# Kernel tuning notes

Measured on AMD Instinct MI355X. Metric: run time of the kernel, lower is better.

## Reference

```python
import jax, jax.numpy as jnp
import numpy as np

N_NODES = 100000
N_EDGES = 1600000
D_IN, D_HID, D_OUT = 128, 256, 128


def setup_inputs() -> dict:
    key = jax.random.key(0)
    ks = jax.random.split(key, 9)
    s = lambda d: 1.0 / np.sqrt(d)
    x = jax.random.normal(ks[0], (N_NODES, D_IN), dtype=jnp.float32)
    edge_index = jax.random.randint(ks[1], (2, N_EDGES), 0, N_NODES, dtype=jnp.int64)
    return {
        "x": x,
        "edge_index": edge_index,
        "Wl1": jax.random.normal(ks[2], (D_IN, D_HID), jnp.float32) * s(D_IN),
        "Wr1": jax.random.normal(ks[3], (D_IN, D_HID), jnp.float32) * s(D_IN),
        "b1": jnp.zeros((D_HID,), jnp.float32),
        "Wl2": jax.random.normal(ks[4], (D_HID, D_HID), jnp.float32) * s(D_HID),
        "Wr2": jax.random.normal(ks[5], (D_HID, D_HID), jnp.float32) * s(D_HID),
        "b2": jnp.zeros((D_HID,), jnp.float32),
        "Wl3": jax.random.normal(ks[6], (D_HID, D_OUT), jnp.float32) * s(D_HID),
        "Wr3": jax.random.normal(ks[7], (D_HID, D_OUT), jnp.float32) * s(D_HID),
        "b3": jnp.zeros((D_OUT,), jnp.float32),
    }


def _sage_conv(x, src, dst, Wl, Wr, b):
    # PyG SAGEConv (mean aggr): out = lin_l(mean_{j in N(i)} x_j) + lin_r(x_i)
    msg = x[src]                                                  # [E, d] gather
    agg = jax.ops.segment_sum(msg, dst, num_segments=N_NODES)    # [N, d] scatter-add
    cnt = jax.ops.segment_sum(jnp.ones((src.shape[0],), x.dtype), dst,
                              num_segments=N_NODES)
    mean = agg / jnp.maximum(cnt, 1.0)[:, None]
    return mean @ Wl + x @ Wr + b


def reference(x, edge_index, Wl1, Wr1, b1, Wl2, Wr2, b2, Wl3, Wr3, b3):
    src, dst = edge_index[0], edge_index[1]
    h = jax.nn.relu(_sage_conv(x, src, dst, Wl1, Wr1, b1))
    h = jax.nn.relu(_sage_conv(h, src, dst, Wl2, Wr2, b2))
    h = jax.nn.relu(_sage_conv(h, src, dst, Wl3, Wr3, b3))
    return h
```

## Files before the change

### kernel.cpp

```cpp
#include <hip/hip_runtime.h>
#include <hip/hip_bf16.h>

#define N_NODES 100000
#define NBUK 391
#define CHUNK 4096

typedef unsigned short ushort_t;
typedef unsigned char uchar_t;
typedef __attribute__((ext_vector_type(8))) short bf16x8;
typedef __attribute__((ext_vector_type(4))) float f32x4;
typedef __attribute__((ext_vector_type(2))) float f32x2;

__device__ inline float bfbits2f(unsigned int lo16) { return __uint_as_float(lo16 << 16); }

__device__ inline ushort_t f2bfbits(float f) {
    __hip_bfloat16 h = __float2bfloat16(f);
    return *reinterpret_cast<ushort_t*>(&h);
}

__device__ inline unsigned int pk2bf(float lo, float hi) {
    return (unsigned int)f2bfbits(lo) | ((unsigned int)f2bfbits(hi) << 16);
}

__device__ inline uchar_t f2fp8(float f) {
    int p = __builtin_amdgcn_cvt_pk_fp8_f32(f, 0.0f, 0, false);
    return (uchar_t)(p & 0xff);
}

__device__ inline void acc8_fp8(float* a, unsigned int ux, unsigned int uy) {
    f32x2 f01 = __builtin_amdgcn_cvt_pk_f32_fp8(ux, false);
    f32x2 f23 = __builtin_amdgcn_cvt_pk_f32_fp8(ux, true);
    f32x2 f45 = __builtin_amdgcn_cvt_pk_f32_fp8(uy, false);
    f32x2 f67 = __builtin_amdgcn_cvt_pk_f32_fp8(uy, true);
    a[0] += f01.x; a[1] += f01.y; a[2] += f23.x; a[3] += f23.y;
    a[4] += f45.x; a[5] += f45.y; a[6] += f67.x; a[7] += f67.y;
}

__device__ inline void acc16_fp8(float* a, uint4 u) {
    acc8_fp8(a, u.x, u.y);
    acc8_fp8(a + 8, u.z, u.w);
}

__global__ __launch_bounds__(256) void scan1(const int* __restrict__ in, int* __restrict__ out,
                                             int* __restrict__ bsum, int n) {
    __shared__ int lds[256];
    const int t = threadIdx.x;
    const int base = blockIdx.x * 1024 + t * 4;
    int4 v = {0, 0, 0, 0};
    if (base + 3 < n) v = *(const int4*)(in + base);
    else {
        v.x = (base + 0 < n) ? in[base + 0] : 0;
        v.y = (base + 1 < n) ? in[base + 1] : 0;
        v.z = (base + 2 < n) ? in[base + 2] : 0;
        v.w = (base + 3 < n) ? in[base + 3] : 0;
    }
    int s0 = v.x, s1 = s0 + v.y, s2 = s1 + v.z, s3 = s2 + v.w;
    lds[t] = s3;
    __syncthreads();
    for (int off = 1; off < 256; off <<= 1) {
        int a = (t >= off) ? lds[t - off] : 0;
        __syncthreads();
        lds[t] += a;
        __syncthreads();
    }
    const int texcl = lds[t] - s3;
    if (t == 255) bsum[blockIdx.x] = lds[255];
    if (base + 0 < n) out[base + 0] = texcl;
    if (base + 1 < n) out[base + 1] = texcl + s0;
    if (base + 2 < n) out[base + 2] = texcl + s1;
    if (base + 3 < n) out[base + 3] = texcl + s2;
}

__global__ __launch_bounds__(256) void scan2(int* __restrict__ bsum, int nb) {
    __shared__ int lds[256];
    const int t = threadIdx.x;
    int v = (t < nb) ? bsum[t] : 0;
    lds[t] = v;
    __syncthreads();
    for (int off = 1; off < 256; off <<= 1) {
        int a = (t >= off) ? lds[t - off] : 0;
        __syncthreads();
        lds[t] += a;
        __syncthreads();
    }
    if (t < nb) bsum[t] = lds[t] - v;
}

__global__ void scan3(int* __restrict__ out, const int* __restrict__ bsum, int n, int E) {
    int i = blockIdx.x * blockDim.x + threadIdx.x;
    if (i < n) out[i] += bsum[i >> 10];
    if (i == 0) out[n] = E;
}

__global__ __launch_bounds__(256) void hist1(const int* __restrict__ dst, int* __restrict__ H,
                                             int E, int NC) {
    __shared__ int h[NBUK + 1];
    const int t = threadIdx.x, c = blockIdx.x;
    for (int g = t; g <= NBUK; g += 256) h[g] = 0;
    __syncthreads();
    const long base = (long)c * CHUNK;
#pragma unroll 4
    for (int it = 0; it < CHUNK / 256; ++it) {
        long e = base + it * 256 + t;
        if (e < E) atomicAdd(&h[((unsigned)dst[e]) >> 8], 1);
    }
    __syncthreads();
    for (int g = t; g < NBUK; g += 256) H[(size_t)g * NC + c] = h[g];
}

__global__ __launch_bounds__(256) void binA(const int* __restrict__ src,
                                            const int* __restrict__ dst,
                                            const int* __restrict__ Hs,
                                            uint2* __restrict__ tmp, int E, int NC) {
    __shared__ int cur[NBUK + 1];
    const int t = threadIdx.x, c = blockIdx.x;
    for (int g = t; g < NBUK; g += 256) cur[g] = Hs[(size_t)g * NC + c];
    __syncthreads();
    const long cb = (long)c * CHUNK;
#pragma unroll 4
    for (int it = 0; it < CHUNK / 256; ++it) {
        long e = cb + it * 256 + t;
        if (e < E) {
            unsigned d = (unsigned)dst[e];
            int pos = atomicAdd(&cur[d >> 8], 1);
            uint2 p = {d, (unsigned)src[e]};
            tmp[pos] = p;
        }
    }
}

__global__ __launch_bounds__(256) void hist2_inv(const uint2* __restrict__ tmp,
                                                 const int* __restrict__ Hs,
                                                 int* __restrict__ cnt,
                                                 float* __restrict__ invd, int NC) {
    __shared__ int h[256];
    const int t = threadIdx.x, b = blockIdx.x;
    h[t] = 0;
    __syncthreads();
    const int beg = Hs[(size_t)b * NC], end = Hs[(size_t)(b + 1) * NC];
    for (int e = beg + t; e < end; e += 256) atomicAdd(&h[tmp[e].x & 255u], 1);
    __syncthreads();
    const int d = b * 256 + t;
    if (d < N_NODES) {
        cnt[d] = h[t];
        invd[d] = 1.0f / (float)max(h[t], 1);
    }
}

__global__ __launch_bounds__(256) void scatter2(const uint2* __restrict__ tmp,
                                                const int* __restrict__ Hs,
                                                const int* __restrict__ roff,
                                                int* __restrict__ csr, int NC) {
    __shared__ int cur[256];
    const int t = threadIdx.x, b = blockIdx.x;
    const int d = b * 256 + t;
    cur[t] = (d <= N_NODES) ? roff[min(d, N_NODES)] : 0;
    __syncthreads();
    const int beg = Hs[(size_t)b * NC], end = Hs[(size_t)(b + 1) * NC];
    for (int e = beg + t; e < end; e += 256) {
        uint2 p = tmp[e];
        int pos = atomicAdd(&cur[p.x & 255u], 1);
        csr[pos] = (int)p.y;
    }
}

__global__ void round_both(const float* __restrict__ x, ushort_t* __restrict__ xb,
                           uchar_t* __restrict__ x8, long n) {
    long i = ((long)blockIdx.x * blockDim.x + threadIdx.x) * 4;
    if (i < n) {
        float4 v = *(const float4*)(x + i);
        ushort4 o = {f2bfbits(v.x), f2bfbits(v.y), f2bfbits(v.z), f2bfbits(v.w)};
        *(ushort4*)(xb + i) = o;
        int w = __builtin_amdgcn_cvt_pk_fp8_f32(v.x, v.y, 0, false);
        w = __builtin_amdgcn_cvt_pk_fp8_f32(v.z, v.w, w, true);
        *(unsigned int*)(x8 + i) = (unsigned int)w;
    }
}

__global__ void cvt_transpose(const float* __restrict__ W, ushort_t* __restrict__ WT,
                              int K, int J, int kdst0, int ldwt) {
    int idx = blockIdx.x * blockDim.x + threadIdx.x;
    if (idx >= K * J) return;
    int k = idx / J, j = idx - k * J;
    WT[(size_t)j * ldwt + kdst0 + k] = f2bfbits(W[idx]);
}

__global__ void cvt6(const float* __restrict__ Wl2, const float* __restrict__ Wr2,
                     const float* __restrict__ Wl3, const float* __restrict__ Wr3,
                     ushort_t* __restrict__ WT2A, ushort_t* __restrict__ WT2B,
                     ushort_t* __restrict__ WT3) {
    const int y = blockIdx.y;
    int idx = blockIdx.x * blockDim.x + threadIdx.x;
    if (idx >= 256 * 128) return;
    int k = idx >> 7, jj = idx & 127;
    const float* W;
    ushort_t* WT;
    int J = 256, jsrc0 = 0;
    switch (y) {
        case 0: W = Wl2; WT = WT2A; break;
        case 1: W = Wr2; WT = WT2A; break;
        case 2: W = Wl2; WT = WT2B; jsrc0 = 128; break;
        case 3: W = Wr2; WT = WT2B; jsrc0 = 128; break;
        case 4: W = Wl3; WT = WT3; J = 128; break;
        default: W = Wr3; WT = WT3; J = 128; break;
    }
    const int row0 = (y & 1) * 128;
    WT[(size_t)(row0 + jj) * 256 + k] = f2bfbits(W[(size_t)k * J + jsrc0 + jj]);
}

template <bool ADDZ, typename OT>
__global__ __launch_bounds__(256) void gather_mean(const uchar_t* __restrict__ Y,
                                                   const ushort_t* __restrict__ Z,
                                                   const int* __restrict__ roff,
                                                   const int* __restrict__ csr,
                                                   const float* __restrict__ invd,
                                                   OT* __restrict__ out, int out_ld, int col0) {
    const int w = (blockIdx.x * blockDim.x + threadIdx.x) >> 6;
    if (w >= N_NODES) return;
    const int lane = threadIdx.x & 63;
    const int g = lane >> 4;
    const int l = lane & 15;
    const int e0 = roff[w], e1 = roff[w + 1];

    float a[8] = {0.f, 0.f, 0.f, 0.f, 0.f, 0.f, 0.f, 0.f};

    int e = e0 + g;
    for (; e + 12 < e1; e += 16) {
        const int s0 = csr[e], s1 = csr[e + 4], s2 = csr[e + 8], s3 = csr[e + 12];
        uint2 u0 = *(const uint2*)(Y + (size_t)s0 * 128 + l * 8);
        uint2 u1 = *(const uint2*)(Y + (size_t)s1 * 128 + l * 8);
        uint2 u2 = *(const uint2*)(Y + (size_t)s2 * 128 + l * 8);
        uint2 u3 = *(const uint2*)(Y + (size_t)s3 * 128 + l * 8);
        acc8_fp8(a, u0.x, u0.y); acc8_fp8(a, u1.x, u1.y);
        acc8_fp8(a, u2.x, u2.y); acc8_fp8(a, u3.x, u3.y);
    }
    for (; e < e1; e += 4) {
        uint2 u0 = *(const uint2*)(Y + (size_t)csr[e] * 128 + l * 8);
        acc8_fp8(a, u0.x, u0.y);
    }

#pragma unroll
    for (int i = 0; i < 8; ++i) {
        a[i] += __shfl_xor(a[i], 16);
        a[i] += __shfl_xor(a[i], 32);
    }

    if (g != 0) return;
    const float iv = invd[w];
#pragma unroll
    for (int i = 0; i < 8; ++i) a[i] *= iv;

    if constexpr (ADDZ) {
        uint4 z = *(const uint4*)(Z + (size_t)w * 128 + l * 8);
        float zf[8];
        zf[0] = bfbits2f(z.x & 0xffffu); zf[1] = __uint_as_float(z.x & 0xffff0000u);
        zf[2] = bfbits2f(z.y & 0xffffu); zf[3] = __uint_as_float(z.y & 0xffff0000u);
        zf[4] = bfbits2f(z.z & 0xffffu); zf[5] = __uint_as_float(z.z & 0xffff0000u);
        zf[6] = bfbits2f(z.w & 0xffffu); zf[7] = __uint_as_float(z.w & 0xffff0000u);
#pragma unroll
        for (int i = 0; i < 8; ++i) a[i] = fmaxf(a[i] + zf[i], 0.0f);
    }

    if constexpr (sizeof(OT) == 4) {
        float* op = (float*)out + (size_t)w * out_ld + col0 + l * 8;
        float4 s0 = {a[0], a[1], a[2], a[3]};
        float4 s1 = {a[4], a[5], a[6], a[7]};
        *(float4*)op = s0;
        *(float4*)(op + 4) = s1;
    } else {
        ushort_t* op = (ushort_t*)out + (size_t)w * out_ld + col0 + l * 8;
        ushort4 lohi0 = {f2bfbits(a[0]), f2bfbits(a[1]), f2bfbits(a[2]), f2bfbits(a[3])};
        ushort4 lohi1 = {f2bfbits(a[4]), f2bfbits(a[5]), f2bfbits(a[6]), f2bfbits(a[7])};
        *(ushort4*)op = lohi0;
        *(ushort4*)(op + 4) = lohi1;
    }
}

__global__ __launch_bounds__(256) void gather256(const uchar_t* __restrict__ Y,
                                                 const ushort_t* __restrict__ Z,
                                                 const int* __restrict__ roff,
                                                 const int* __restrict__ csr,
                                                 const float* __restrict__ invd,
                                                 ushort_t* __restrict__ out) {
    const int w = (blockIdx.x * blockDim.x + threadIdx.x) >> 6;
    if (w >= N_NODES) return;
    const int lane = threadIdx.x & 63;
    const int g = lane >> 4;
    const int l = lane & 15;
    const int e0 = roff[w], e1 = roff[w + 1];

    float a[16];
#pragma unroll
    for (int i = 0; i < 16; ++i) a[i] = 0.0f;

    int e = e0 + g;
    for (; e + 12 < e1; e += 16) {
        const int s0 = csr[e], s1 = csr[e + 4], s2 = csr[e + 8], s3 = csr[e + 12];
        uint4 u0 = *(const uint4*)(Y + (size_t)s0 * 256 + l * 16);
        uint4 u1 = *(const uint4*)(Y + (size_t)s1 * 256 + l * 16);
        uint4 u2 = *(const uint4*)(Y + (size_t)s2 * 256 + l * 16);
        uint4 u3 = *(const uint4*)(Y + (size_t)s3 * 256 + l * 16);
        acc16_fp8(a, u0); acc16_fp8(a, u1); acc16_fp8(a, u2); acc16_fp8(a, u3);
    }
    for (; e < e1; e += 4) {
        uint4 u0 = *(const uint4*)(Y + (size_t)csr[e] * 256 + l * 16);
        acc16_fp8(a, u0);
    }

#pragma unroll
    for (int i = 0; i < 16; ++i) {
        a[i] += __shfl_xor(a[i], 16);
        a[i] += __shfl_xor(a[i], 32);
    }

    if (g != 0) return;
    const float iv = invd[w];

    uint4 z0 = *(const uint4*)(Z + (size_t)w * 256 + l * 16);
    uint4 z1 = *(const uint4*)(Z + (size_t)w * 256 + l * 16 + 8);
    float zf[16];
    zf[0] = bfbits2f(z0.x & 0xffffu);  zf[1] = __uint_as_float(z0.x & 0xffff0000u);
    zf[2] = bfbits2f(z0.y & 0xffffu);  zf[3] = __uint_as_float(z0.y & 0xffff0000u);
    zf[4] = bfbits2f(z0.z & 0xffffu);  zf[5] = __uint_as_float(z0.z & 0xffff0000u);
    zf[6] = bfbits2f(z0.w & 0xffffu);  zf[7] = __uint_as_float(z0.w & 0xffff0000u);
    zf[8] = bfbits2f(z1.x & 0xffffu);  zf[9] = __uint_as_float(z1.x & 0xffff0000u);
    zf[10] = bfbits2f(z1.y & 0xffffu); zf[11] = __uint_as_float(z1.y & 0xffff0000u);
    zf[12] = bfbits2f(z1.z & 0xffffu); zf[13] = __uint_as_float(z1.z & 0xffff0000u);
    zf[14] = bfbits2f(z1.w & 0xffffu); zf[15] = __uint_as_float(z1.w & 0xffff0000u);

#pragma unroll
    for (int i = 0; i < 16; ++i) a[i] = fmaxf(a[i] * iv + zf[i], 0.0f);

    ushort_t* op = out + (size_t)w * 256 + l * 16;
    uint4 s0, s1;
    s0.x = pk2bf(a[0], a[1]);   s0.y = pk2bf(a[2], a[3]);
    s0.z = pk2bf(a[4], a[5]);   s0.w = pk2bf(a[6], a[7]);
    s1.x = pk2bf(a[8], a[9]);   s1.y = pk2bf(a[10], a[11]);
    s1.z = pk2bf(a[12], a[13]); s1.w = pk2bf(a[14], a[15]);
    *(uint4*)op = s0;
    *(uint4*)(op + 8) = s1;
}

template <int KH, bool CONCAT, int MODE>
__global__ __launch_bounds__(256) void mfma_gemm256(const ushort_t* __restrict__ A,
                                                    const ushort_t* __restrict__ A2,
                                                    const ushort_t* __restrict__ WT,
                                                    const float* __restrict__ bias,
                                                    void* __restrict__ out0p, int ld0,
                                                    ushort_t* __restrict__ out1, int ld1) {
    constexpr int KTOT = CONCAT ? 2 * KH : KH;
    constexpr int BK = 32;
    constexpr int NT = KTOT / BK;
    __shared__ ushort_t smem[2][12288];

    const int tid = threadIdx.x;
    const int lane = tid & 63;
    const int w = tid >> 6;
    const int wr = w >> 1, wc = w & 1;
    const int n0 = blockIdx.x * 128;

    const int srow = lane >> 2;
    const int skc = (lane & 3) ^ ((srow >> 1) & 3);

    f32x4 acc0[4][4], acc1[4][4];
#pragma unroll
    for (int m = 0; m < 4; ++m)
#pragma unroll
        for (int n = 0; n < 4; ++n) {
            acc0[m][n] = (f32x4){0.f, 0.f, 0.f, 0.f};
            acc1[m][n] = (f32x4){0.f, 0.f, 0.f, 0.f};
        }

    auto STAGE = [&](int b, int t) {
        const int k0 = t * BK;
        const ushort_t* Asrc = A;
        int ak = k0;
        if (CONCAT && k0 >= KH) { Asrc = A2; ak = k0 - KH; }
#pragma unroll
        for (int i = 0; i < 2; ++i) {
            const int ci = w * 2 + i;
            int grow = n0 + ci * 16 + srow;
            grow = min(grow, N_NODES - 1);
            const ushort_t* g = Asrc + (size_t)grow * KH + ak + skc * 8;
            __builtin_amdgcn_global_load_lds((const unsigned int*)g,
                                             (unsigned int*)(&smem[b][ci * 512]), 16, 0, 0);
        }
#pragma unroll
        for (int i = 0; i < 4; ++i) {
            const int ci = w * 4 + i;
            const int jrow = ci * 16 + srow;
            const ushort_t* g = WT + (size_t)jrow * KTOT + k0 + skc * 8;
            __builtin_amdgcn_global_load_lds((const unsigned int*)g,
                                             (unsigned int*)(&smem[b][4096 + ci * 512]), 16, 0, 0);
        }
    };

    auto COMPUTE = [&](int b) {
        const int kc = lane >> 4;
        bf16x8 af[4], b0[4], b1[4];
#pragma unroll
        for (int m = 0; m < 4; ++m) {
            const int row = wr * 64 + m * 16 + (lane & 15);
            const int slot = kc ^ ((row >> 1) & 3);
            af[m] = *(const bf16x8*)((const char*)&smem[b][0] + row * 64 + slot * 16);
        }
#pragma unroll
        for (int n = 0; n < 4; ++n) {
            const int r0 = wc * 64 + n * 16 + (lane & 15);
            const int r1 = 128 + r0;
            const int s0 = kc ^ ((r0 >> 1) & 3);
            const int s1 = kc ^ ((r1 >> 1) & 3);
            b0[n] = *(const bf16x8*)((const char*)&smem[b][4096] + r0 * 64 + s0 * 16);
            b1[n] = *(const bf16x8*)((const char*)&smem[b][4096] + r1 * 64 + s1 * 16);
        }
#pragma unroll
        for (int m = 0; m < 4; ++m)
#pragma unroll
            for (int n = 0; n < 4; ++n) {
                acc0[m][n] = __builtin_amdgcn_mfma_f32_16x16x32_bf16(af[m], b0[n],
                                                                     acc0[m][n], 0, 0, 0);
                acc1[m][n] = __builtin_amdgcn_mfma_f32_16x16x32_bf16(af[m], b1[n],
                                                                     acc1[m][n], 0, 0, 0);
            }
    };

    STAGE(0, 0);
    __syncthreads();
    int cur = 0;
#pragma unroll
    for (int t = 0; t < NT - 1; ++t) {
        STAGE(cur ^ 1, t + 1);
        COMPUTE(cur);
        __syncthreads();
        cur ^= 1;
    }
    COMPUTE(cur);

    const int c15 = lane & 15;
    const int r4 = (lane >> 4) * 4;
#pragma unroll
    for (int m = 0; m < 4; ++m) {
#pragma unroll
        for (int q = 0; q < 4; ++q) {
            const int row_g = n0 + wr * 64 + m * 16 + r4 + q;
            if (row_g >= N_NODES) continue;
#pragma unroll
            for (int n = 0; n < 4; ++n) {
                const int lcol = wc * 64 + n * 16 + c15;
                const float v0 = acc0[m][n][q];
                const float v1 = acc1[m][n][q];
                if constexpr (MODE == 0) {
                    ushort_t* o = (ushort_t*)out0p;
                    o[(size_t)row_g * ld0 + lcol] = f2bfbits(fmaxf(v0 + bias[lcol], 0.0f));
                    o[(size_t)row_g * ld0 + 128 + lcol] =
                        f2bfbits(fmaxf(v1 + bias[128 + lcol], 0.0f));
                } else {
                    ((uchar_t*)out0p)[(size_t)row_g * ld0 + lcol] = f2fp8(v0);
                    out1[(size_t)row_g * ld1 + lcol] = f2bfbits(v1 + bias[lcol]);
                }
            }
        }
    }
}

extern "C" void kernel_launch(void* const* d_in, const int* in_sizes, int n_in,
                              void* d_out, int out_size, void* d_ws, size_t ws_size,
                              hipStream_t stream) {
    const float* x   = (const float*)d_in[0];
    const int*   ei  = (const int*)d_in[1];
    const float* Wl1 = (const float*)d_in[2];
    const float* Wr1 = (const float*)d_in[3];
    const float* b1  = (const float*)d_in[4];
    const float* Wl2 = (const float*)d_in[5];
    const float* Wr2 = (const float*)d_in[6];
    const float* b2  = (const float*)d_in[7];
    const float* Wl3 = (const float*)d_in[8];
    const float* Wr3 = (const float*)d_in[9];
    const float* b3  = (const float*)d_in[10];

    const int E = in_sizes[1] / 2;
    const int* src = ei;
    const int* dst = ei + E;
    const int N = N_NODES;
    const int NC = (E + CHUNK - 1) / CHUNK;
    const int nH = NBUK * NC;

    char* ws = (char*)d_ws;
    float* invd = (float*)(ws + 0);
    int* cnt    = (int*)(ws + 400000);
    int* roff   = (int*)(ws + 800000);
    int* bsum   = (int*)(ws + 1200016);
    int* H      = (int*)(ws + 1201040);
    ushort_t* WT1  = (ushort_t*)(ws + 1812568);
    ushort_t* WT2A = (ushort_t*)(ws + 1943640);
    ushort_t* WT2B = (ushort_t*)(ws + 2074712);
    ushort_t* WT3  = (ushort_t*)(ws + 2205784);
    uint2* tmp  = (uint2*)(ws + 2336864);
    int* csr    = (int*)(ws + 15136864);
    ushort_t* h1 = (ushort_t*)(ws + 21536864);
    ushort_t* h2 = (ushort_t*)(ws + 72736864);
    ushort_t* M1 = h2;
    ushort_t* T1 = (ushort_t*)(ws + 123936864);
    const size_t WS_NEED = 149536864;
    if (ws_size < WS_NEED) return;

    uchar_t* T8  = (uchar_t*)tmp;
    uchar_t* T1a = (uchar_t*)T1;
    ushort_t* Zd = (ushort_t*)d_out;
    ushort_t* Zh = h1;

    const int GX = (N + 127) / 128;
    const int NBH = (nH + 1023) / 1024;
    const int NBN = (N + 1023) / 1024;

    hist1<<<NC, 256, 0, stream>>>(dst, H, E, NC);
    scan1<<<NBH, 256, 0, stream>>>(H, H, bsum, nH);
    scan2<<<1, 256, 0, stream>>>(bsum, NBH);
    scan3<<<(nH + 256) / 256, 256, 0, stream>>>(H, bsum, nH, E);
    binA<<<NC, 256, 0, stream>>>(src, dst, H, tmp, E, NC);
    hist2_inv<<<NBUK, 256, 0, stream>>>(tmp, H, cnt, invd, NC);
    scan1<<<NBN, 256, 0, stream>>>(cnt, roff, bsum, N);
    scan2<<<1, 256, 0, stream>>>(bsum, NBN);
    scan3<<<(N + 256) / 256, 256, 0, stream>>>(roff, bsum, N, E);
    scatter2<<<NBUK, 256, 0, stream>>>(tmp, H, roff, csr, NC);

    cvt_transpose<<<(128 * 256 + 255) / 256, 256, 0, stream>>>(Wl1, WT1, 128, 256, 0, 256);
    cvt_transpose<<<(128 * 256 + 255) / 256, 256, 0, stream>>>(Wr1, WT1, 128, 256, 128, 256);
    cvt6<<<dim3(128, 6), 256, 0, stream>>>(Wl2, Wr2, Wl3, Wr3, WT2A, WT2B, WT3);

    round_both<<<(N * 128 / 4 + 255) / 256, 256, 0, stream>>>(x, T1, T8, (long)N * 128);
    gather_mean<false, ushort_t><<<(N * 64 + 255) / 256, 256, 0, stream>>>(
        T8, nullptr, roff, csr, invd, M1, 128, 0);
    mfma_gemm256<128, true, 0><<<GX, 256, 0, stream>>>(
        M1, T1, WT1, b1, h1, 256, nullptr, 0);

    mfma_gemm256<256, false, 1><<<GX, 256, 0, stream>>>(
        h1, nullptr, WT2A, b2 + 0, T1a, 256, Zd, 256);
    mfma_gemm256<256, false, 1><<<GX, 256, 0, stream>>>(
        h1, nullptr, WT2B, b2 + 128, T1a + 128, 256, Zd + 128, 256);
    gather256<<<(N * 64 + 255) / 256, 256, 0, stream>>>(
        T1a, Zd, roff, csr, invd, h2);

    mfma_gemm256<256, false, 1><<<GX, 256, 0, stream>>>(
        h2, nullptr, WT3, b3, T8, 128, Zh, 128);
    gather_mean<true, float><<<(N * 64 + 255) / 256, 256, 0, stream>>>(
        T8, Zh, roff, csr, invd, (float*)d_out, 128, 0);
}
```

Before: 447.4 us.

## Split neighbor gathers into 32-column slices processed by interleaved blocks

Replaces the per-node gather kernels with one templated kernel in which each wavefront handles a 32-byte column slice of a node, and consecutive blocks cover the different slices of the same node group. The intent is to shrink each pass's working set, so concurrent blocks touching the same slice share cache lines in L2/MALL and gather locality improves. The cost is more wavefronts, with every slice re-reading the CSR indices and offsets. Each lane now issues small 4-byte loads, and a third shuffle-reduction step is added.

```diff
diff --git a/kernel.cpp b/kernel.cpp
--- a/kernel.cpp
+++ b/kernel.cpp
@@ -18,27 +18,15 @@
     return *reinterpret_cast<ushort_t*>(&h);
 }
 
-__device__ inline unsigned int pk2bf(float lo, float hi) {
-    return (unsigned int)f2bfbits(lo) | ((unsigned int)f2bfbits(hi) << 16);
-}
-
 __device__ inline uchar_t f2fp8(float f) {
     int p = __builtin_amdgcn_cvt_pk_fp8_f32(f, 0.0f, 0, false);
     return (uchar_t)(p & 0xff);
 }
 
-__device__ inline void acc8_fp8(float* a, unsigned int ux, unsigned int uy) {
-    f32x2 f01 = __builtin_amdgcn_cvt_pk_f32_fp8(ux, false);
-    f32x2 f23 = __builtin_amdgcn_cvt_pk_f32_fp8(ux, true);
-    f32x2 f45 = __builtin_amdgcn_cvt_pk_f32_fp8(uy, false);
-    f32x2 f67 = __builtin_amdgcn_cvt_pk_f32_fp8(uy, true);
+__device__ inline void acc4_fp8(float* a, unsigned int u) {
+    f32x2 f01 = __builtin_amdgcn_cvt_pk_f32_fp8(u, false);
+    f32x2 f23 = __builtin_amdgcn_cvt_pk_f32_fp8(u, true);
     a[0] += f01.x; a[1] += f01.y; a[2] += f23.x; a[3] += f23.y;
-    a[4] += f45.x; a[5] += f45.y; a[6] += f67.x; a[7] += f67.y;
-}
-
-__device__ inline void acc16_fp8(float* a, uint4 u) {
-    acc8_fp8(a, u.x, u.y);
-    acc8_fp8(a + 8, u.z, u.w);
 }
 
 __global__ __launch_bounds__(256) void scan1(const int* __restrict__ in, int* __restrict__ out,
@@ -208,137 +196,69 @@
     WT[(size_t)(row0 + jj) * 256 + k] = f2bfbits(W[(size_t)k * J + jsrc0 + jj]);
 }
 
-template <bool ADDZ, typename OT>
-__global__ __launch_bounds__(256) void gather_mean(const uchar_t* __restrict__ Y,
-                                                   const ushort_t* __restrict__ Z,
-                                                   const int* __restrict__ roff,
-                                                   const int* __restrict__ csr,
-                                                   const float* __restrict__ invd,
-                                                   OT* __restrict__ out, int out_ld, int col0) {
-    const int w = (blockIdx.x * blockDim.x + threadIdx.x) >> 6;
-    if (w >= N_NODES) return;
-    const int lane = threadIdx.x & 63;
-    const int g = lane >> 4;
-    const int l = lane & 15;
-    const int e0 = roff[w], e1 = roff[w + 1];
-
-    float a[8] = {0.f, 0.f, 0.f, 0.f, 0.f, 0.f, 0.f, 0.f};
-
-    int e = e0 + g;
-    for (; e + 12 < e1; e += 16) {
-        const int s0 = csr[e], s1 = csr[e + 4], s2 = csr[e + 8], s3 = csr[e + 12];
-        uint2 u0 = *(const uint2*)(Y + (size_t)s0 * 128 + l * 8);
-        uint2 u1 = *(const uint2*)(Y + (size_t)s1 * 128 + l * 8);
-        uint2 u2 = *(const uint2*)(Y + (size_t)s2 * 128 + l * 8);
-        uint2 u3 = *(const uint2*)(Y + (size_t)s3 * 128 + l * 8);
-        acc8_fp8(a, u0.x, u0.y); acc8_fp8(a, u1.x, u1.y);
-        acc8_fp8(a, u2.x, u2.y); acc8_fp8(a, u3.x, u3.y);
-    }
-    for (; e < e1; e += 4) {
-        uint2 u0 = *(const uint2*)(Y + (size_t)csr[e] * 128 + l * 8);
-        acc8_fp8(a, u0.x, u0.y);
-    }
-
-#pragma unroll
-    for (int i = 0; i < 8; ++i) {
-        a[i] += __shfl_xor(a[i], 16);
-        a[i] += __shfl_xor(a[i], 32);
-    }
-
-    if (g != 0) return;
-    const float iv = invd[w];
-#pragma unroll
-    for (int i = 0; i < 8; ++i) a[i] *= iv;
-
-    if constexpr (ADDZ) {
-        uint4 z = *(const uint4*)(Z + (size_t)w * 128 + l * 8);
-        float zf[8];
-        zf[0] = bfbits2f(z.x & 0xffffu); zf[1] = __uint_as_float(z.x & 0xffff0000u);
-        zf[2] = bfbits2f(z.y & 0xffffu); zf[3] = __uint_as_float(z.y & 0xffff0000u);
-        zf[4] = bfbits2f(z.z & 0xffffu); zf[5] = __uint_as_float(z.z & 0xffff0000u);
-        zf[6] = bfbits2f(z.w & 0xffffu); zf[7] = __uint_as_float(z.w & 0xffff0000u);
-#pragma unroll
-        for (int i = 0; i < 8; ++i) a[i] = fmaxf(a[i] + zf[i], 0.0f);
-    }
-
-    if constexpr (sizeof(OT) == 4) {
-        float* op = (float*)out + (size_t)w * out_ld + col0 + l * 8;
-        float4 s0 = {a[0], a[1], a[2], a[3]};
-        float4 s1 = {a[4], a[5], a[6], a[7]};
-        *(float4*)op = s0;
-        *(float4*)(op + 4) = s1;
-    } else {
-        ushort_t* op = (ushort_t*)out + (size_t)w * out_ld + col0 + l * 8;
-        ushort4 lohi0 = {f2bfbits(a[0]), f2bfbits(a[1]), f2bfbits(a[2]), f2bfbits(a[3])};
-        ushort4 lohi1 = {f2bfbits(a[4]), f2bfbits(a[5]), f2bfbits(a[6]), f2bfbits(a[7])};
-        *(ushort4*)op = lohi0;
-        *(ushort4*)(op + 4) = lohi1;
-    }
-}
-
-__global__ __launch_bounds__(256) void gather256(const uchar_t* __restrict__ Y,
+template <int NCOLS, bool ADDZ, typename OT>
+__global__ __launch_bounds__(256) void gather_sl(const uchar_t* __restrict__ Y,
                                                  const ushort_t* __restrict__ Z,
                                                  const int* __restrict__ roff,
                                                  const int* __restrict__ csr,
                                                  const float* __restrict__ invd,
-                                                 ushort_t* __restrict__ out) {
-    const int w = (blockIdx.x * blockDim.x + threadIdx.x) >> 6;
-    if (w >= N_NODES) return;
+                                                 OT* __restrict__ out) {
+    const int bx = blockIdx.x;
+    const int s8 = bx & 7;
+    int slice, ng;
+    if (NCOLS == 256) { slice = s8; ng = bx >> 3; }
+    else { slice = s8 & 3; ng = ((bx >> 3) << 1) | (s8 >> 2); }
+
+    const int node = ng * 4 + (threadIdx.x >> 6);
+    if (node >= N_NODES) return;
     const int lane = threadIdx.x & 63;
-    const int g = lane >> 4;
-    const int l = lane & 15;
-    const int e0 = roff[w], e1 = roff[w + 1];
-
-    float a[16];
-#pragma unroll
-    for (int i = 0; i < 16; ++i) a[i] = 0.0f;
+    const int g = lane >> 3;
+    const int li = lane & 7;
+    const int e0 = roff[node], e1 = roff[node + 1];
+    const size_t coff = (size_t)slice * 32 + li * 4;
+
+    float a[4] = {0.f, 0.f, 0.f, 0.f};
 
     int e = e0 + g;
-    for (; e + 12 < e1; e += 16) {
-        const int s0 = csr[e], s1 = csr[e + 4], s2 = csr[e + 8], s3 = csr[e + 12];
-        uint4 u0 = *(const uint4*)(Y + (size_t)s0 * 256 + l * 16);
-        uint4 u1 = *(const uint4*)(Y + (size_t)s1 * 256 + l * 16);
-        uint4 u2 = *(const uint4*)(Y + (size_t)s2 * 256 + l * 16);
-        uint4 u3 = *(const uint4*)(Y + (size_t)s3 * 256 + l * 16);
-        acc16_fp8(a, u0); acc16_fp8(a, u1); acc16_fp8(a, u2); acc16_fp8(a, u3);
-    }
-    for (; e < e1; e += 4) {
-        uint4 u0 = *(const uint4*)(Y + (size_t)csr[e] * 256 + l * 16);
-        acc16_fp8(a, u0);
-    }
-
-#pragma unroll
-    for (int i = 0; i < 16; ++i) {
+    for (; e + 8 < e1; e += 16) {
+        unsigned int u0 = *(const unsigned int*)(Y + (size_t)csr[e] * NCOLS + coff);
+        unsigned int u1 = *(const unsigned int*)(Y + (size_t)csr[e + 8] * NCOLS + coff);
+        acc4_fp8(a, u0);
+        acc4_fp8(a, u1);
+    }
+    if (e < e1) {
+        unsigned int u0 = *(const unsigned int*)(Y + (size_t)csr[e] * NCOLS + coff);
+        acc4_fp8(a, u0);
+    }
+
+#pragma unroll
+    for (int i = 0; i < 4; ++i) {
+        a[i] += __shfl_xor(a[i], 8);
         a[i] += __shfl_xor(a[i], 16);
         a[i] += __shfl_xor(a[i], 32);
     }
 
     if (g != 0) return;
-    const float iv = invd[w];
-
-    uint4 z0 = *(const uint4*)(Z + (size_t)w * 256 + l * 16);
-    uint4 z1 = *(const uint4*)(Z + (size_t)w * 256 + l * 16 + 8);
-    float zf[16];
-    zf[0] = bfbits2f(z0.x & 0xffffu);  zf[1] = __uint_as_float(z0.x & 0xffff0000u);
-    zf[2] = bfbits2f(z0.y & 0xffffu);  zf[3] = __uint_as_float(z0.y & 0xffff0000u);
-    zf[4] = bfbits2f(z0.z & 0xffffu);  zf[5] = __uint_as_float(z0.z & 0xffff0000u);
-    zf[6] = bfbits2f(z0.w & 0xffffu);  zf[7] = __uint_as_float(z0.w & 0xffff0000u);
-    zf[8] = bfbits2f(z1.x & 0xffffu);  zf[9] = __uint_as_float(z1.x & 0xffff0000u);
-    zf[10] = bfbits2f(z1.y & 0xffffu); zf[11] = __uint_as_float(z1.y & 0xffff0000u);
-    zf[12] = bfbits2f(z1.z & 0xffffu); zf[13] = __uint_as_float(z1.z & 0xffff0000u);
-    zf[14] = bfbits2f(z1.w & 0xffffu); zf[15] = __uint_as_float(z1.w & 0xffff0000u);
-
-#pragma unroll
-    for (int i = 0; i < 16; ++i) a[i] = fmaxf(a[i] * iv + zf[i], 0.0f);
-
-    ushort_t* op = out + (size_t)w * 256 + l * 16;
-    uint4 s0, s1;
-    s0.x = pk2bf(a[0], a[1]);   s0.y = pk2bf(a[2], a[3]);
-    s0.z = pk2bf(a[4], a[5]);   s0.w = pk2bf(a[6], a[7]);
-    s1.x = pk2bf(a[8], a[9]);   s1.y = pk2bf(a[10], a[11]);
-    s1.z = pk2bf(a[12], a[13]); s1.w = pk2bf(a[14], a[15]);
-    *(uint4*)op = s0;
-    *(uint4*)(op + 8) = s1;
+    const float iv = invd[node];
+#pragma unroll
+    for (int i = 0; i < 4; ++i) a[i] *= iv;
+
+    if constexpr (ADDZ) {
+        uint2 z = *(const uint2*)(Z + (size_t)node * NCOLS + slice * 32 + li * 4);
+        float zf[4];
+        zf[0] = bfbits2f(z.x & 0xffffu); zf[1] = __uint_as_float(z.x & 0xffff0000u);
+        zf[2] = bfbits2f(z.y & 0xffffu); zf[3] = __uint_as_float(z.y & 0xffff0000u);
+#pragma unroll
+        for (int i = 0; i < 4; ++i) a[i] = fmaxf(a[i] + zf[i], 0.0f);
+    }
+
+    if constexpr (sizeof(OT) == 4) {
+        float4 st = {a[0], a[1], a[2], a[3]};
+        *(float4*)((float*)out + (size_t)node * 128 + slice * 32 + li * 4) = st;
+    } else {
+        ushort4 st = {f2bfbits(a[0]), f2bfbits(a[1]), f2bfbits(a[2]), f2bfbits(a[3])};
+        *(ushort4*)((ushort_t*)out + (size_t)node * NCOLS + slice * 32 + li * 4) = st;
+    }
 }
 
 template <int KH, bool CONCAT, int MODE>
@@ -512,6 +432,8 @@
     const int GX = (N + 127) / 128;
     const int NBH = (nH + 1023) / 1024;
     const int NBN = (N + 1023) / 1024;
+    const int G128 = 8 * ((N + 7) / 8);
+    const int G256 = 8 * ((N + 3) / 4);
 
     hist1<<<NC, 256, 0, stream>>>(dst, H, E, NC);
     scan1<<<NBH, 256, 0, stream>>>(H, H, bsum, nH);
@@ -529,8 +451,8 @@
     cvt6<<<dim3(128, 6), 256, 0, stream>>>(Wl2, Wr2, Wl3, Wr3, WT2A, WT2B, WT3);
 
     round_both<<<(N * 128 / 4 + 255) / 256, 256, 0, stream>>>(x, T1, T8, (long)N * 128);
-    gather_mean<false, ushort_t><<<(N * 64 + 255) / 256, 256, 0, stream>>>(
-        T8, nullptr, roff, csr, invd, M1, 128, 0);
+    gather_sl<128, false, ushort_t><<<G128, 256, 0, stream>>>(
+        T8, nullptr, roff, csr, invd, M1);
     mfma_gemm256<128, true, 0><<<GX, 256, 0, stream>>>(
         M1, T1, WT1, b1, h1, 256, nullptr, 0);
 
@@ -538,11 +460,11 @@
         h1, nullptr, WT2A, b2 + 0, T1a, 256, Zd, 256);
     mfma_gemm256<256, false, 1><<<GX, 256, 0, stream>>>(
         h1, nullptr, WT2B, b2 + 128, T1a + 128, 256, Zd + 128, 256);
-    gather256<<<(N * 64 + 255) / 256, 256, 0, stream>>>(
+    gather_sl<256, true, ushort_t><<<G256, 256, 0, stream>>>(
         T1a, Zd, roff, csr, invd, h2);
 
     mfma_gemm256<256, false, 1><<<GX, 256, 0, stream>>>(
         h2, nullptr, WT3, b3, T8, 128, Zh, 128);
-    gather_mean<true, float><<<(N * 64 + 255) / 256, 256, 0, stream>>>(
-        T8, Zh, roff, csr, invd, (float*)d_out, 128, 0);
-}
+    gather_sl<128, true, float><<<G128, 256, 0, stream>>>(
+        T8, Zh, roff, csr, invd, (float*)d_out);
+}
```

After: 792.6 us. 77.2% more time.
